# Kernel tuning notes

Measured on AMD Instinct MI355X. Metric: run time of the kernel, lower is better.

The kernel has to match this reference:

```python
import jax, jax.numpy as jnp
import numpy as np

KP_EXTENT = 0.05
N_Q = 40000   # query points
N_S = 40000   # support points
K = 32        # neighbors per query
P = 15        # kernel points
IN_DIM = 64
OUT_DIM = 128


def setup_inputs() -> dict:
    key = jax.random.key(0)
    k1, k2, k3, k4, k5, k6 = jax.random.split(key, 6)
    q_pts = jax.random.uniform(k1, (N_Q, 3), dtype=jnp.float32)
    s_pts = jax.random.uniform(k2, (N_S, 3), dtype=jnp.float32)
    # indices in [0, N_S]; value N_S hits the appended shadow row
    neighbor_idxs = jax.random.randint(k3, (N_Q, K), 0, N_S + 1)
    x = jax.random.normal(k4, (N_S, IN_DIM), dtype=jnp.float32)
    weights = jax.random.normal(k5, (P, IN_DIM, OUT_DIM), dtype=jnp.float32) * 0.05
    kernel_points = jax.random.normal(k6, (P, 3), dtype=jnp.float32) * 0.06
    return {"q_pts": q_pts, "s_pts": s_pts, "neighbor_idxs": neighbor_idxs,
            "x": x, "weights": weights, "kernel_points": kernel_points}


def reference(q_pts, s_pts, neighbor_idxs, x, weights, kernel_points):
    # Append shadow support point. NOTE: the original does
    # zeros_like(s_pts[:1,:] + 1e6) which is exactly zeros, so shadow = origin.
    s_pad = jnp.concatenate([s_pts, jnp.zeros_like(s_pts[:1, :])], axis=0)
    # Gather neighbor coordinates, center on queries: [N, K, 3]
    neighbors = s_pad[neighbor_idxs] - q_pts[:, None, :]
    # Distances to every kernel point: [N, K, P]
    diff = neighbors[:, :, None, :] - kernel_points[None, None, :, :]
    sq_distances = jnp.sum(diff * diff, axis=3)
    all_weights = jnp.clip(1.0 - jnp.sqrt(sq_distances) / KP_EXTENT, 0.0)
    all_weights = jnp.transpose(all_weights, (0, 2, 1))  # [N, P, K]
    # Gather neighbor features with zero shadow row: [N, K, D_in]
    feats = jnp.concatenate([x, jnp.zeros_like(x[:1, :])], axis=0)
    neighbors_x = feats[neighbor_idxs]
    # Kernel-point weighted aggregation: [N, P, D_in] -> [P, N, D_in]
    weighted_features = jnp.transpose(jnp.matmul(all_weights, neighbors_x), (1, 0, 2))
    # Per-kernel-point linear map: [P, N, D_out], then sum over kernel points
    kernel_outputs = jnp.matmul(weighted_features, weights)
    output_features = jnp.sum(kernel_outputs, axis=0)  # [N, D_out]
    # Normalize by count of "valid" neighbors (feature-sum > 0 heuristic)
    neighbor_features_sum = jnp.sum(neighbors_x, axis=-1)          # [N, K]
    neighbor_num = jnp.sum(neighbor_features_sum > 0.0, axis=-1)   # [N]
    neighbor_num = jnp.maximum(neighbor_num, 1).astype(output_features.dtype)
    return output_features / neighbor_num[:, None]
```

## Files before the change

### kernel.cpp

```cpp
#include <hip/hip_runtime.h>

#define N_Q     40000
#define N_S     40000
#define KK      32
#define PP      15
#define IN_DIM  64
#define OUT_DIM 128

__global__ __launch_bounds__(256) void rowsum_valid_kernel(
    const float* __restrict__ x, int* __restrict__ valid) {
  int t = blockIdx.x * 256 + threadIdx.x;
  int row = t >> 4;
  int sub = t & 15;
  if (row >= N_S) return;
  float4 v = reinterpret_cast<const float4*>(x + (size_t)row * IN_DIM)[sub];
  float s = (v.x + v.y) + (v.z + v.w);
  s += __shfl_xor(s, 1, 64);
  s += __shfl_xor(s, 2, 64);
  s += __shfl_xor(s, 4, 64);
  s += __shfl_xor(s, 8, 64);
  if (sub == 0) valid[row] = (s > 0.0f) ? 1 : 0;
}

__global__ __launch_bounds__(256) void kpconv_fused_kernel(
    const float* __restrict__ q_pts, const float* __restrict__ s_pts,
    const int* __restrict__ nidx, const float* __restrict__ x,
    const float* __restrict__ weights, const float* __restrict__ kpts,
    const int* __restrict__ valid, float* __restrict__ out) {
  const int tid  = blockIdx.x * 256 + threadIdx.x;
  const int lane = threadIdx.x & 63;
  const int n  = tid >> 5;
  const int nA = (tid & ~63) >> 5;

  float kx[PP], ky[PP], kz[PP];
  #pragma unroll
  for (int p = 0; p < PP; ++p) {
    kx[p] = kpts[p * 3 + 0];
    ky[p] = kpts[p * 3 + 1];
    kz[p] = kpts[p * 3 + 2];
  }

  const int id = nidx[tid];
  const bool real = (id < N_S);
  float ox = 0.f, oy = 0.f, oz = 0.f;
  int v = 0;
  if (real) {
    ox = s_pts[id * 3 + 0];
    oy = s_pts[id * 3 + 1];
    oz = s_pts[id * 3 + 2];
    v  = valid[id];
  }
  ox -= q_pts[n * 3 + 0];
  oy -= q_pts[n * 3 + 1];
  oz -= q_pts[n * 3 + 2];

  unsigned long long bal = __ballot(v != 0);
  unsigned int half = (lane < 32) ? (unsigned int)bal
                                  : (unsigned int)(bal >> 32);
  int num = (int)__popc(half);
  if (num < 1) num = 1;
  const float invnum = 1.0f / (float)num;

  float a0 = 0.f, a1 = 0.f;
  float b0 = 0.f, b1 = 0.f;

  #pragma unroll
  for (int p = 0; p < PP; ++p) {
    const float dx = ox - kx[p];
    const float dy = oy - ky[p];
    const float dz = oz - kz[p];
    const float d2 = dx * dx + dy * dy + dz * dz;
    const bool hit = real && (d2 < 0.0025f);
    unsigned long long b2 = __ballot(hit);
    if (b2 != 0ull) {
      const float wn = hit ? (1.0f - 20.0f * sqrtf(d2)) * invnum : 0.0f;
      while (b2) {
        const int j = __ffsll(b2) - 1;
        b2 &= b2 - 1;
        const float wj  = __shfl(wn, j);
        const int   idj = __shfl(id, j);
        const float xv = x[(size_t)idj * IN_DIM + lane];
        const float* wp = weights + (size_t)p * IN_DIM * OUT_DIM + 2 * lane;
        float h0 = 0.f, h1 = 0.f;
        #pragma unroll 16
        for (int d = 0; d < IN_DIM; ++d) {
          const float xd = __shfl(xv, d);
          const float2 w2 = *reinterpret_cast<const float2*>(wp + (size_t)d * OUT_DIM);
          h0 += xd * w2.x;
          h1 += xd * w2.y;
        }
        if (j < 32) { a0 += wj * h0; a1 += wj * h1; }
        else        { b0 += wj * h0; b1 += wj * h1; }
      }
    }
  }

  float2 ra; ra.x = a0; ra.y = a1;
  float2 rb; rb.x = b0; rb.y = b1;
  *reinterpret_cast<float2*>(out + (size_t)nA * OUT_DIM + 2 * lane) = ra;
  *reinterpret_cast<float2*>(out + (size_t)(nA + 1) * OUT_DIM + 2 * lane) = rb;
}

extern "C" void kernel_launch(void* const* d_in, const int* in_sizes, int n_in,
                              void* d_out, int out_size, void* d_ws, size_t ws_size,
                              hipStream_t stream) {
  const float* q_pts   = (const float*)d_in[0];
  const float* s_pts   = (const float*)d_in[1];
  const int*   nidx    = (const int*)d_in[2];
  const float* x       = (const float*)d_in[3];
  const float* weights = (const float*)d_in[4];
  const float* kpts    = (const float*)d_in[5];
  float* out = (float*)d_out;
  int* valid = (int*)d_ws;

  rowsum_valid_kernel<<<(N_S * 16) / 256, 256, 0, stream>>>(x, valid);
  kpconv_fused_kernel<<<(N_Q * KK) / 256, 256, 0, stream>>>(
      q_pts, s_pts, nidx, x, weights, kpts, valid, out);
}
```

Measured before the change: 113.1 us.

## Pack support coords with validity flag, convert weights to bf16, broadcast-load x rows

The prep kernel now writes a packed float4 per support point (xyz plus validity flag) with a zero shadow row, and converts the weight tensor to bf16 in workspace. The main kernel does one gather for coordinates and validity, and reads x rows as uniform float4 broadcasts instead of shuffling a per-lane load. This is meant to cut gather and shuffle traffic and halve weight bandwidth. The cost is bf16 rounding of the weights, which adds numerical error.

```diff
diff --git a/kernel.cpp b/kernel.cpp
--- a/kernel.cpp
+++ b/kernel.cpp
@@ -1,4 +1,5 @@
 #include <hip/hip_runtime.h>
+#include <hip/hip_bf16.h>
 
 #define N_Q     40000
 #define N_S     40000
@@ -7,26 +8,49 @@
 #define IN_DIM  64
 #define OUT_DIM 128
 
-__global__ __launch_bounds__(256) void rowsum_valid_kernel(
-    const float* __restrict__ x, int* __restrict__ valid) {
-  int t = blockIdx.x * 256 + threadIdx.x;
-  int row = t >> 4;
-  int sub = t & 15;
-  if (row >= N_S) return;
-  float4 v = reinterpret_cast<const float4*>(x + (size_t)row * IN_DIM)[sub];
-  float s = (v.x + v.y) + (v.z + v.w);
-  s += __shfl_xor(s, 1, 64);
-  s += __shfl_xor(s, 2, 64);
-  s += __shfl_xor(s, 4, 64);
-  s += __shfl_xor(s, 8, 64);
-  if (sub == 0) valid[row] = (s > 0.0f) ? 1 : 0;
+
+__global__ __launch_bounds__(256) void prep_kernel(
+    const float* __restrict__ x, const float* __restrict__ s_pts,
+    const float* __restrict__ weights,
+    float4* __restrict__ packed, __hip_bfloat162* __restrict__ wbf) {
+  const int b = blockIdx.x;
+  if (b < 2500) {
+    const int t = b * 256 + threadIdx.x;
+    const int row = t >> 4;
+    const int sub = t & 15;
+    float4 v = reinterpret_cast<const float4*>(x + (size_t)row * IN_DIM)[sub];
+    float s = (v.x + v.y) + (v.z + v.w);
+    s += __shfl_xor(s, 1, 64);
+    s += __shfl_xor(s, 2, 64);
+    s += __shfl_xor(s, 4, 64);
+    s += __shfl_xor(s, 8, 64);
+    if (sub == 0) {
+      float4 pkt;
+      pkt.x = s_pts[row * 3 + 0];
+      pkt.y = s_pts[row * 3 + 1];
+      pkt.z = s_pts[row * 3 + 2];
+      pkt.w = (s > 0.0f) ? 1.0f : 0.0f;
+      packed[row] = pkt;
+    }
+    if (t == 1) {
+      float4 z; z.x = 0.f; z.y = 0.f; z.z = 0.f; z.w = 0.f;
+      packed[N_S] = z;
+    }
+  } else {
+    const int t = (b - 2500) * 256 + threadIdx.x;
+    float2 w2 = reinterpret_cast<const float2*>(weights)[t];
+    __hip_bfloat162 h;
+    h.x = __float2bfloat16(w2.x);
+    h.y = __float2bfloat16(w2.y);
+    wbf[t] = h;
+  }
 }
 
 __global__ __launch_bounds__(256) void kpconv_fused_kernel(
-    const float* __restrict__ q_pts, const float* __restrict__ s_pts,
-    const int* __restrict__ nidx, const float* __restrict__ x,
-    const float* __restrict__ weights, const float* __restrict__ kpts,
-    const int* __restrict__ valid, float* __restrict__ out) {
+    const float* __restrict__ q_pts, const int* __restrict__ nidx,
+    const float* __restrict__ x, const float* __restrict__ kpts,
+    const float4* __restrict__ packed, const __hip_bfloat162* __restrict__ wbf,
+    float* __restrict__ out) {
   const int tid  = blockIdx.x * 256 + threadIdx.x;
   const int lane = threadIdx.x & 63;
   const int n  = tid >> 5;
@@ -41,20 +65,14 @@
   }
 
   const int id = nidx[tid];
+  const float4 sp = packed[id];
   const bool real = (id < N_S);
-  float ox = 0.f, oy = 0.f, oz = 0.f;
-  int v = 0;
-  if (real) {
-    ox = s_pts[id * 3 + 0];
-    oy = s_pts[id * 3 + 1];
-    oz = s_pts[id * 3 + 2];
-    v  = valid[id];
-  }
-  ox -= q_pts[n * 3 + 0];
-  oy -= q_pts[n * 3 + 1];
-  oz -= q_pts[n * 3 + 2];
 
-  unsigned long long bal = __ballot(v != 0);
+  const float ox = sp.x - q_pts[n * 3 + 0];
+  const float oy = sp.y - q_pts[n * 3 + 1];
+  const float oz = sp.z - q_pts[n * 3 + 2];
+
+  unsigned long long bal = __ballot(sp.w != 0.0f);
   unsigned int half = (lane < 32) ? (unsigned int)bal
                                   : (unsigned int)(bal >> 32);
   int num = (int)__popc(half);
@@ -79,15 +97,23 @@
         b2 &= b2 - 1;
         const float wj  = __shfl(wn, j);
         const int   idj = __shfl(id, j);
-        const float xv = x[(size_t)idj * IN_DIM + lane];
-        const float* wp = weights + (size_t)p * IN_DIM * OUT_DIM + 2 * lane;
+        const float* xr = x + (size_t)idj * IN_DIM;
+        const __hip_bfloat162* wp =
+            wbf + (size_t)p * (IN_DIM * OUT_DIM / 2) + lane;
         float h0 = 0.f, h1 = 0.f;
-        #pragma unroll 16
-        for (int d = 0; d < IN_DIM; ++d) {
-          const float xd = __shfl(xv, d);
-          const float2 w2 = *reinterpret_cast<const float2*>(wp + (size_t)d * OUT_DIM);
-          h0 += xd * w2.x;
-          h1 += xd * w2.y;
+        #pragma unroll 4
+        for (int d4 = 0; d4 < IN_DIM / 4; ++d4) {
+          const float4 xv4 =
+              *reinterpret_cast<const float4*>(xr + 4 * d4);
+          #pragma unroll
+          for (int dd = 0; dd < 4; ++dd) {
+            const int d = 4 * d4 + dd;
+            const __hip_bfloat162 w2 = wp[(size_t)d * (OUT_DIM / 2)];
+            const float xd = (dd == 0) ? xv4.x : (dd == 1) ? xv4.y
+                           : (dd == 2) ? xv4.z : xv4.w;
+            h0 += xd * __bfloat162float(w2.x);
+            h1 += xd * __bfloat162float(w2.y);
+          }
         }
         if (j < 32) { a0 += wj * h0; a1 += wj * h1; }
         else        { b0 += wj * h0; b1 += wj * h1; }
@@ -111,9 +137,12 @@
   const float* weights = (const float*)d_in[4];
   const float* kpts    = (const float*)d_in[5];
   float* out = (float*)d_out;
-  int* valid = (int*)d_ws;
 
-  rowsum_valid_kernel<<<(N_S * 16) / 256, 256, 0, stream>>>(x, valid);
+  char* ws = (char*)d_ws;
+  float4*          packed = (float4*)ws;
+  __hip_bfloat162* wbf    = (__hip_bfloat162*)(ws + (1u << 20));
+
+  prep_kernel<<<2740, 256, 0, stream>>>(x, s_pts, weights, packed, wbf);
   kpconv_fused_kernel<<<(N_Q * KK) / 256, 256, 0, stream>>>(
-      q_pts, s_pts, nidx, x, weights, kpts, valid, out);
+      q_pts, nidx, x, kpts, packed, wbf, out);
 }
```

Result: faster. 105.1 us (-7.1%).
